# Kernel tuning notes

Measured on AMD Instinct MI355X. Metric: run time of the kernel, lower is better.

Reference implementation:

```python
import jax, jax.numpy as jnp
import numpy as np

BRANCH = 16   # children per internal node
DEPTH = 4     # levels 0..4, leaves at level 4
IN = 512
HID = 512

def _level_sizes():
    return [BRANCH ** d for d in range(DEPTH + 1)]

def setup_inputs() -> dict:
    key = jax.random.key(0)
    ks = jax.random.split(key, 9)
    N = sum(_level_sizes())  # 69905
    x = jax.random.normal(ks[0], (N, IN), dtype=jnp.float32)
    s = 1.0 / np.sqrt(IN + HID)  # torch nn.Linear default init bound
    def lin(kw, kb):
        w = jax.random.uniform(kw, (HID, IN + HID), jnp.float32, -s, s)
        b = jax.random.uniform(kb, (HID,), jnp.float32, -s, s)
        return w, b
    wi_w, wi_b = lin(ks[1], ks[2])
    wf_w, wf_b = lin(ks[3], ks[4])
    wo_w, wo_b = lin(ks[5], ks[6])
    wu_w, wu_b = lin(ks[7], ks[8])
    return {"x": x, "wi_w": wi_w, "wi_b": wi_b, "wf_w": wf_w, "wf_b": wf_b,
            "wo_w": wo_w, "wo_b": wo_b, "wu_w": wu_w, "wu_b": wu_b}

def reference(x, wi_w, wi_b, wf_w, wf_b, wo_w, wo_b, wu_w, wu_b):
    sizes = _level_sizes()
    offs = np.concatenate([[0], np.cumsum(sizes)])
    levels = [x[offs[d]:offs[d + 1]] for d in range(DEPTH + 1)]

    def gates(xh):
        i = jax.nn.sigmoid(xh @ wi_w.T + wi_b)
        o = jax.nn.sigmoid(xh @ wo_w.T + wo_b)
        u = jnp.tanh(xh @ wu_w.T + wu_b)
        return i, o, u

    # leaf_forward: h_prev = 0, no forget terms
    Xl = levels[DEPTH]
    xh = jnp.concatenate([Xl, jnp.zeros((Xl.shape[0], HID), Xl.dtype)], axis=1)
    i, o, u = gates(xh)
    C = i * u
    H = o * jnp.tanh(C)

    # node_forward, bottom-up. Faithful quirk of the source: the forget gate
    # is computed on the child CELL state (cat(x, c_k)), not the hidden state.
    for d in range(DEPTH - 1, -1, -1):
        Xd = levels[d]                      # [n, IN]
        n = Xd.shape[0]
        Hc = H.reshape(n, BRANCH, HID)      # children hidden
        Cc = C.reshape(n, BRANCH, HID)      # children cell
        h_sum = Hc.sum(axis=1)
        xh = jnp.concatenate([Xd, h_sum], axis=1)
        i, o, u = gates(xh)
        xc = jnp.concatenate([jnp.broadcast_to(Xd[:, None, :], (n, BRANCH, IN)), Cc], axis=-1)
        f = jax.nn.sigmoid(jnp.einsum('nbk,hk->nbh', xc, wf_w) + wf_b)
        C = i * u + (f * Cc).sum(axis=1)
        H = o * jnp.tanh(C)

    return H[0], C[0]
```

## Files before the change

### kernel.cpp

```cpp
#include <hip/hip_runtime.h>
#include <stdint.h>
#include <stddef.h>


typedef __bf16 bf16x8 __attribute__((ext_vector_type(8)));
typedef float  f32x4  __attribute__((ext_vector_type(4)));
typedef void __attribute__((address_space(3))) lds_void_t;
typedef void __attribute__((address_space(1))) gbl_void_t;

__device__ __forceinline__ uint16_t f2bf(float f) {
  union { __bf16 b; uint16_t u; } v;
  v.b = (__bf16)f;
  return v.u;
}
__device__ __forceinline__ float bf2f(uint16_t u) {
  union { uint32_t u; float f; } v; v.u = (uint32_t)u << 16;
  return v.f;
}
__device__ __forceinline__ float sig_(float x) {
  return __builtin_amdgcn_rcpf(1.0f + __expf(-x));
}
__device__ __forceinline__ float tanh_(float x) {
  return __builtin_fmaf(2.f,
      __builtin_amdgcn_rcpf(1.f + __expf(-2.f * x)), -1.f);
}

__global__ void k_conv_all(const float4* __restrict__ x,
                           ushort4* __restrict__ xdst, long n4x,
                           const float4* __restrict__ w0,
                           const float4* __restrict__ w1,
                           const float4* __restrict__ w2,
                           const float4* __restrict__ w3,
                           ushort4* __restrict__ wdst) {
  const long per4 = (long)512 * 1024 / 4;
  const long total = n4x + 4 * per4;
  long i = blockIdx.x * (long)blockDim.x + threadIdx.x;
  long stride = (long)gridDim.x * blockDim.x;
  for (; i < total; i += stride) {
    float4 v;
    ushort4* d;
    if (i < n4x) {
      v = x[i];
      d = xdst + i;
    } else {
      long j = i - n4x;
      long seg = j / per4, off2 = j - seg * per4;
      const float4* s = (seg == 0) ? w0 : (seg == 1) ? w1
                       : (seg == 2) ? w2 : w3;
      v = s[off2];
      d = wdst + j;
    }
    ushort4 r;
    r.x = f2bf(v.x); r.y = f2bf(v.y); r.z = f2bf(v.z); r.w = f2bf(v.w);
    *d = r;
  }
}

#define BM 128
#define BN 128
#define BK 32

__global__ __launch_bounds__(256)
void k_gemm_bt(const uint16_t* __restrict__ A, int lda,
               const uint16_t* __restrict__ B, int ldb,
               float* __restrict__ C, int ldc, int K) {
  __shared__ uint16_t As[BM * BK];
  __shared__ uint16_t Bs[BN * BK];
  const int tid = threadIdx.x, lane = tid & 63, wave = tid >> 6;
  const int lrow = lane & 15, quad = lane >> 4;
  const int wm = (wave >> 1) * 64, wn = (wave & 1) * 64;
  const long tm = blockIdx.x, tn = blockIdx.y;
  f32x4 acc[4][4] = {};
  const int srow = lane >> 2, scol = (lane & 3) * 8;
  for (int k0 = 0; k0 < K; k0 += BK) {
#pragma unroll
    for (int i = 0; i < 2; ++i) {
      int row = i * 64 + wave * 16 + srow;
      const uint16_t* gp = A + (tm * BM + row) * (long)lda + k0 + scol;
      __builtin_amdgcn_global_load_lds((gbl_void_t*)(uintptr_t)gp,
          (lds_void_t*)&As[i * 2048 + wave * 512], 16, 0, 0);
    }
#pragma unroll
    for (int i = 0; i < 2; ++i) {
      int row = i * 64 + wave * 16 + srow;
      const uint16_t* gp = B + (tn * BN + row) * (long)ldb + k0 + scol;
      __builtin_amdgcn_global_load_lds((gbl_void_t*)(uintptr_t)gp,
          (lds_void_t*)&Bs[i * 2048 + wave * 512], 16, 0, 0);
    }
    __syncthreads();
    bf16x8 a[4], b[4];
#pragma unroll
    for (int f = 0; f < 4; ++f)
      a[f] = *(const bf16x8*)&As[(wm + f * 16 + lrow) * BK + quad * 8];
#pragma unroll
    for (int f = 0; f < 4; ++f)
      b[f] = *(const bf16x8*)&Bs[(wn + f * 16 + lrow) * BK + quad * 8];
#pragma unroll
    for (int fm = 0; fm < 4; ++fm)
#pragma unroll
      for (int fn = 0; fn < 4; ++fn)
        acc[fm][fn] = __builtin_amdgcn_mfma_f32_16x16x32_bf16(
            a[fm], b[fn], acc[fm][fn], 0, 0, 0);
    __syncthreads();
  }
#pragma unroll
  for (int fm = 0; fm < 4; ++fm)
#pragma unroll
    for (int fn = 0; fn < 4; ++fn) {
      long col  = tn * BN + wn + fn * 16 + lrow;
      long row0 = tm * BM + wm + fm * 16 + quad * 4;
#pragma unroll
      for (int r = 0; r < 4; ++r)
        C[(row0 + r) * (long)ldc + col] = acc[fm][fn][r];
    }
}

template <bool HAS_F>
__global__ __launch_bounds__(256, 3)
void k_level(const uint16_t* __restrict__ A, int lda, int K,
             const uint16_t* __restrict__ Wg,
             const float* __restrict__ bi, const float* __restrict__ bo,
             const float* __restrict__ bu,
             const float* __restrict__ Fpart,
             uint16_t* __restrict__ Cbf,
             const uint16_t* __restrict__ Xnext,
             uint16_t* __restrict__ xh_next) {
  __shared__ uint16_t As[128 * 64];
  __shared__ uint16_t Bs[192 * 64];
  const int tid = threadIdx.x, lane = tid & 63, wave = tid >> 6;
  const int lrow = lane & 15, quad = lane >> 4;
  const int wm = (wave >> 1) * 64, wn = (wave & 1) * 32;

  long tm, tn;
  {
    const int nTm = (int)(gridDim.x >> 3);
    int b = blockIdx.x;
    if ((nTm & 7) == 0) {
      int x = b & 7, j = b >> 3, per = nTm >> 3;
      tn = j & 7; tm = (long)x * per + (j >> 3);
    } else { tm = b >> 3; tn = b & 7; }
  }

  f32x4 acc[3][4][2] = {};

  const int srow = lane >> 3;
  const int scol = (((lane & 7) ^ srow) << 3);
  const int rsw = lrow & 7;
  const int pc[2] = { ((0 + quad) ^ rsw) << 3, ((4 + quad) ^ rsw) << 3 };

  for (int k0 = 0; k0 < K; k0 += 64) {
#pragma unroll
    for (int j = 0; j < 4; ++j) {
      int row = wave * 32 + j * 8 + srow;
      const uint16_t* gp = A + (tm * 128 + row) * (long)lda + k0 + scol;
      __builtin_amdgcn_global_load_lds((gbl_void_t*)(uintptr_t)gp,
          (lds_void_t*)&As[(wave * 32 + j * 8) * 64], 16, 0, 0);
    }
#pragma unroll
    for (int j = 0; j < 6; ++j) {
      int cc = wave * 6 + j;
      int g  = cc >> 3;
      long grow = (long)g * 512 + tn * 64 + (cc & 7) * 8 + srow;
      const uint16_t* gp = Wg + grow * 1024 + k0 + scol;
      __builtin_amdgcn_global_load_lds((gbl_void_t*)(uintptr_t)gp,
          (lds_void_t*)&Bs[cc * 512], 16, 0, 0);
    }
    __syncthreads();

#pragma unroll
    for (int h = 0; h < 2; ++h) {
      bf16x8 a[4];
#pragma unroll
      for (int f = 0; f < 4; ++f)
        a[f] = *(const bf16x8*)&As[(wm + f * 16 + lrow) * 64 + pc[h]];
#pragma unroll
      for (int g = 0; g < 3; ++g) {
        bf16x8 b0 = *(const bf16x8*)&Bs[(g * 64 + wn + lrow) * 64 + pc[h]];
        bf16x8 b1 = *(const bf16x8*)&Bs[(g * 64 + wn + 16 + lrow) * 64 +
                                        pc[h]];
#pragma unroll
        for (int fm = 0; fm < 4; ++fm) {
          acc[g][fm][0] = __builtin_amdgcn_mfma_f32_16x16x32_bf16(
              a[fm], b0, acc[g][fm][0], 0, 0, 0);
          acc[g][fm][1] = __builtin_amdgcn_mfma_f32_16x16x32_bf16(
              a[fm], b1, acc[g][fm][1], 0, 0, 0);
        }
      }
    }
    __syncthreads();
  }

#pragma unroll
  for (int fn = 0; fn < 2; ++fn) {
    long col = tn * 64 + wn + fn * 16 + lrow;
    float biv = bi[col], bov = bo[col], buv = bu[col];
#pragma unroll
    for (int fm = 0; fm < 4; ++fm) {
      long row0 = tm * 128 + wm + fm * 16 + quad * 4;
      long pg   = tm * 8 + (wm >> 4) + fm;
      float hs = 0.f;
#pragma unroll
      for (int r = 0; r < 4; ++r) {
        long row = row0 + r;
        float iv = sig_(acc[0][fm][fn][r] + biv);
        float ov = sig_(acc[1][fm][fn][r] + bov);
        float uv = tanh_(acc[2][fm][fn][r] + buv);
        float c  = iv * uv;
        if (HAS_F) c += Fpart[row * 512 + col];
        Cbf[row * 512 + col] = f2bf(c);
        hs += ov * tanh_(c);
      }
      hs += __shfl_xor(hs, 16, 64);
      hs += __shfl_xor(hs, 32, 64);
      if (quad == 0) {
        xh_next[pg * 1024 + col]       = Xnext[pg * 512 + col];
        xh_next[pg * 1024 + 512 + col] = f2bf(hs);
      }
    }
  }
}

__global__ __launch_bounds__(256, 3)
void k_fc_combine(const uint16_t* __restrict__ Cbf,
                  const uint16_t* __restrict__ Wfc, int ldb,
                  const float* __restrict__ Fx,
                  const float* __restrict__ bfb,
                  float* __restrict__ Fpart) {
  __shared__ uint16_t As[128 * 64];
  __shared__ uint16_t Bs[128 * 64];
  const int tid = threadIdx.x, lane = tid & 63, wave = tid >> 6;
  const int lrow = lane & 15, quad = lane >> 4;
  const int wm = (wave >> 1) * 64, wn = (wave & 1) * 64;
  long tm, tn;
  {
    const int nTm = (int)(gridDim.x >> 2);
    int b = blockIdx.x;
    if ((nTm & 7) == 0) {
      int x = b & 7, j = b >> 3, per = nTm >> 3;
      tn = j & 3; tm = (long)x * per + (j >> 2);
    } else { tm = b >> 2; tn = b & 3; }
  }
  const int lda = 512;
  f32x4 acc[4][4] = {};

  const int srow = lane >> 3;
  const int scol = (((lane & 7) ^ srow) << 3);
  const int rsw = lrow & 7;
  const int pc[2] = { ((0 + quad) ^ rsw) << 3, ((4 + quad) ^ rsw) << 3 };

  for (int k0 = 0; k0 < 512; k0 += 64) {
#pragma unroll
    for (int j = 0; j < 4; ++j) {
      int row = wave * 32 + j * 8 + srow;
      const uint16_t* gp = Cbf + (tm * BM + row) * (long)lda + k0 + scol;
      __builtin_amdgcn_global_load_lds((gbl_void_t*)(uintptr_t)gp,
          (lds_void_t*)&As[(wave * 32 + j * 8) * 64], 16, 0, 0);
    }
#pragma unroll
    for (int j = 0; j < 4; ++j) {
      int row = wave * 32 + j * 8 + srow;
      const uint16_t* gp = Wfc + (tn * BN + row) * (long)ldb + k0 + scol;
      __builtin_amdgcn_global_load_lds((gbl_void_t*)(uintptr_t)gp,
          (lds_void_t*)&Bs[(wave * 32 + j * 8) * 64], 16, 0, 0);
    }
    __syncthreads();
#pragma unroll
    for (int h = 0; h < 2; ++h) {
      bf16x8 a[4], b[4];
#pragma unroll
      for (int f = 0; f < 4; ++f)
        a[f] = *(const bf16x8*)&As[(wm + f * 16 + lrow) * 64 + pc[h]];
#pragma unroll
      for (int f = 0; f < 4; ++f)
        b[f] = *(const bf16x8*)&Bs[(wn + f * 16 + lrow) * 64 + pc[h]];
#pragma unroll
      for (int fm = 0; fm < 4; ++fm)
#pragma unroll
        for (int fn = 0; fn < 4; ++fn)
          acc[fm][fn] = __builtin_amdgcn_mfma_f32_16x16x32_bf16(
              a[fm], b[fn], acc[fm][fn], 0, 0, 0);
    }
    __syncthreads();
  }
#pragma unroll
  for (int fm = 0; fm < 4; ++fm) {
    long pg   = tm * 8 + (wm >> 4) + fm;
    long row0 = tm * BM + wm + fm * 16 + quad * 4;
#pragma unroll
    for (int fn = 0; fn < 4; ++fn) {
      long col = tn * BN + wn + fn * 16 + lrow;
      float fx = Fx[pg * 512 + col] + bfb[col];
      float t = 0.f;
#pragma unroll
      for (int r = 0; r < 4; ++r)
        t += sig_(fx + acc[fm][fn][r]) * bf2f(Cbf[(row0 + r) * 512 + col]);
      t += __shfl_xor(t, 16, 64);
      t += __shfl_xor(t, 32, 64);
      if (quad == 0) Fpart[pg * 512 + col] = t;
    }
  }
}

__global__ void k_dot_bb(const uint16_t* __restrict__ A, int lda,
                         const uint16_t* __restrict__ B, int ldb,
                         float* __restrict__ C, int ldc,
                         int M, int N, int K) {
  int wid  = (int)((blockIdx.x * (long)blockDim.x + threadIdx.x) >> 6);
  int lane = threadIdx.x & 63;
  if (wid >= M * N) return;
  int m = wid / N, n = wid - m * N;
  const uint16_t* a = A + (long)m * lda;
  const uint16_t* b = B + (long)n * ldb;
  int per = K >> 6, k0 = lane * per;
  float s = 0.f;
  for (int j = 0; j < per; j += 4) {
    ushort4 av = *(const ushort4*)(a + k0 + j);
    ushort4 bv = *(const ushort4*)(b + k0 + j);
    s += bf2f(av.x) * bf2f(bv.x) + bf2f(av.y) * bf2f(bv.y)
       + bf2f(av.z) * bf2f(bv.z) + bf2f(av.w) * bf2f(bv.w);
  }
#pragma unroll
  for (int off = 32; off; off >>= 1) s += __shfl_xor(s, off, 64);
  if (lane == 0) C[(long)m * ldc + n] = s;
}
__global__ void k_dot_f32(const float* __restrict__ A, int lda,
                          const float* __restrict__ B, int ldb,
                          float* __restrict__ C, int ldc,
                          int M, int N, int K) {
  int wid  = (int)((blockIdx.x * (long)blockDim.x + threadIdx.x) >> 6);
  int lane = threadIdx.x & 63;
  if (wid >= M * N) return;
  int m = wid / N, n = wid - m * N;
  const float* a = A + (long)m * lda;
  const float* b = B + (long)n * ldb;
  int per = K >> 6, k0 = lane * per;
  float s = 0.f;
  for (int j = 0; j < per; j += 4) {
    float4 av = *(const float4*)(a + k0 + j);
    float4 bv = *(const float4*)(b + k0 + j);
    s += av.x * bv.x + av.y * bv.y + av.z * bv.z + av.w * bv.w;
  }
#pragma unroll
  for (int off = 32; off; off >>= 1) s += __shfl_xor(s, off, 64);
  if (lane == 0) C[(long)m * ldc + n] = s;
}

__global__ void k_hsum_xh4(const float* __restrict__ Hc,
                           const uint16_t* __restrict__ xd,
                           uint16_t* __restrict__ xh, int n) {
  long idx = blockIdx.x * (long)blockDim.x + threadIdx.x;
  if (idx >= (long)n * 128) return;
  long p = idx >> 7; int hq = (int)(idx & 127) << 2;
  const float* hp = Hc + (p << 4) * 512 + hq;
  float4 s = {0.f, 0.f, 0.f, 0.f};
#pragma unroll
  for (int b = 0; b < 16; ++b) {
    float4 v = *(const float4*)(hp + b * 512);
    s.x += v.x; s.y += v.y; s.z += v.z; s.w += v.w;
  }
  *(ushort4*)(xh + p * 1024 + hq) = *(const ushort4*)(xd + p * 512 + hq);
  ushort4 hw = {f2bf(s.x), f2bf(s.y), f2bf(s.z), f2bf(s.w)};
  *(ushort4*)(xh + p * 1024 + 512 + hq) = hw;
}

__global__ void k_final4(const float* __restrict__ G,
                         const float* __restrict__ Fpart,
                         const float* __restrict__ bi,
                         const float* __restrict__ bo,
                         const float* __restrict__ bu,
                         float* __restrict__ H, float* __restrict__ Cv,
                         uint16_t* __restrict__ Cbf, int n) {
  long idx = blockIdx.x * (long)blockDim.x + threadIdx.x;
  if (idx >= (long)n * 128) return;
  long p = idx >> 7; int hq = (int)(idx & 127) << 2;
  const float* g = G + p * 1536;
  float4 gi = *(const float4*)(g + hq);
  float4 go = *(const float4*)(g + 512 + hq);
  float4 gu = *(const float4*)(g + 1024 + hq);
  float4 b_i = *(const float4*)(bi + hq);
  float4 b_o = *(const float4*)(bo + hq);
  float4 b_u = *(const float4*)(bu + hq);
  float4 fp = *(const float4*)(Fpart + p * 512 + hq);
  const float* gip = &gi.x; const float* gop = &go.x; const float* gup = &gu.x;
  const float* bip = &b_i.x; const float* bop = &b_o.x; const float* bup = &b_u.x;
  const float* fpp = &fp.x;
  float4 hv, cv;
  float* hvp = &hv.x; float* cvp = &cv.x;
  ushort4 cw; unsigned short* cwp = &cw.x;
#pragma unroll
  for (int j = 0; j < 4; ++j) {
    float iv = sig_(gip[j] + bip[j]);
    float ov = sig_(gop[j] + bop[j]);
    float uv = tanh_(gup[j] + bup[j]);
    float c  = iv * uv + fpp[j];
    cvp[j] = c;
    cwp[j] = f2bf(c);
    hvp[j] = ov * tanh_(c);
  }
  *(float4*)(H  + p * 512 + hq) = hv;
  *(float4*)(Cv + p * 512 + hq) = cv;
  *(ushort4*)(Cbf + p * 512 + hq) = cw;
}

__global__ void k_root_tail(const float* __restrict__ Fc,
                            const float* __restrict__ Fx,
                            const float* __restrict__ bfb,
                            const float* __restrict__ Cc,
                            const float* __restrict__ G,
                            const float* __restrict__ bi,
                            const float* __restrict__ bo,
                            const float* __restrict__ bu,
                            float* __restrict__ H, float* __restrict__ Cv) {
  int hq = (threadIdx.x & 127) << 2;
  float4 fxv = *(const float4*)(Fx + hq);
  float4 bfv = *(const float4*)(bfb + hq);
  float fx0 = fxv.x + bfv.x, fx1 = fxv.y + bfv.y;
  float fx2 = fxv.z + bfv.z, fx3 = fxv.w + bfv.w;
  float a0 = 0.f, a1 = 0.f, a2 = 0.f, a3 = 0.f;
#pragma unroll 4
  for (int b = 0; b < 16; ++b) {
    float4 f = *(const float4*)(Fc + (long)b * 512 + hq);
    float4 c = *(const float4*)(Cc + (long)b * 512 + hq);
    a0 += sig_(fx0 + f.x) * c.x;
    a1 += sig_(fx1 + f.y) * c.y;
    a2 += sig_(fx2 + f.z) * c.z;
    a3 += sig_(fx3 + f.w) * c.w;
  }
  float fpp[4] = {a0, a1, a2, a3};
  float4 gi = *(const float4*)(G + hq);
  float4 go = *(const float4*)(G + 512 + hq);
  float4 gu = *(const float4*)(G + 1024 + hq);
  float4 b_i = *(const float4*)(bi + hq);
  float4 b_o = *(const float4*)(bo + hq);
  float4 b_u = *(const float4*)(bu + hq);
  const float* gip = &gi.x; const float* gop = &go.x; const float* gup = &gu.x;
  const float* bip = &b_i.x; const float* bop = &b_o.x; const float* bup = &b_u.x;
  float4 hv, cv;
  float* hvp = &hv.x; float* cvp = &cv.x;
#pragma unroll
  for (int j = 0; j < 4; ++j) {
    float iv = sig_(gip[j] + bip[j]);
    float ov = sig_(gop[j] + bop[j]);
    float uv = tanh_(gup[j] + bup[j]);
    float c  = iv * uv + fpp[j];
    cvp[j] = c;
    hvp[j] = ov * tanh_(c);
  }
  *(float4*)(H  + hq) = hv;
  *(float4*)(Cv + hq) = cv;
}

extern "C" void kernel_launch(void* const* d_in, const int* in_sizes, int n_in,
                              void* d_out, int out_size, void* d_ws, size_t ws_size,
                              hipStream_t stream) {
  const float* x    = (const float*)d_in[0];
  const float* wi_w = (const float*)d_in[1];
  const float* wi_b = (const float*)d_in[2];
  const float* wf_w = (const float*)d_in[3];
  const float* wf_b = (const float*)d_in[4];
  const float* wo_w = (const float*)d_in[5];
  const float* wo_b = (const float*)d_in[6];
  const float* wu_w = (const float*)d_in[7];
  const float* wu_b = (const float*)d_in[8];
  (void)in_sizes; (void)n_in; (void)out_size; (void)ws_size;

  static const long offs[5] = {0, 1, 17, 273, 4369};
  const long NTOT = 69905;

  char* ws = (char*)d_ws;
  size_t off = 0;
  auto alloc = [&](size_t bytes) -> void* {
    void* p = ws + off;
    off += (bytes + 255) & ~(size_t)255;
    return p;
  };
  uint16_t* Xbf   = (uint16_t*)alloc(NTOT * 512 * 2);
  uint16_t* Wgw   = (uint16_t*)alloc((size_t)2048 * 1024 * 2);
  uint16_t* Wg    = Wgw;
  uint16_t* Wf    = Wgw + (size_t)1536 * 1024;
  float*    FxAll = (float*)alloc((size_t)4480 * 512 * 4);
  uint16_t* Cbf   = (uint16_t*)alloc((size_t)65536 * 512 * 2);
  uint16_t* CbfU  = (uint16_t*)alloc((size_t)4096 * 512 * 2);
  uint16_t* CbfU2 = (uint16_t*)alloc((size_t)256 * 512 * 2);
  uint16_t* xhA   = (uint16_t*)alloc((size_t)4096 * 1024 * 2);
  uint16_t* xhB   = (uint16_t*)alloc((size_t)256 * 1024 * 2);
  uint16_t* xhC   = (uint16_t*)alloc((size_t)16 * 1024 * 2);
  float*    Fpart = (float*)alloc((size_t)4096 * 512 * 4);
  float*    Gf    = (float*)alloc((size_t)16 * 1536 * 4);
  float*    Fc    = (float*)alloc((size_t)16 * 512 * 4);
  float*    HupA  = (float*)alloc((size_t)16 * 512 * 4);
  float*    CupA  = (float*)alloc((size_t)16 * 512 * 4);

  auto blks = [](long n) { return (int)((n + 255) / 256); };

  {
    long n4x = NTOT * 512 / 4;
    k_conv_all<<<8192, 256, 0, stream>>>(
        (const float4*)x, (ushort4*)Xbf, n4x,
        (const float4*)wi_w, (const float4*)wo_w,
        (const float4*)wu_w, (const float4*)wf_w, (ushort4*)Wgw);
  }

  {
    dim3 grid(35, 4);
    k_gemm_bt<<<grid, 256, 0, stream>>>(Xbf, 512, Wf, 1024, FxAll, 512, 512);
  }

  k_level<false><<<4096, 256, 0, stream>>>(
      Xbf + offs[4] * 512, 512, 512, Wg, wi_b, wo_b, wu_b, nullptr,
      Cbf, Xbf + offs[3] * 512, xhA);
  k_fc_combine<<<2048, 256, 0, stream>>>(Cbf, Wf + 512, 1024,
                                         FxAll + offs[3] * 512, wf_b, Fpart);

  k_level<true><<<256, 256, 0, stream>>>(
      xhA, 1024, 1024, Wg, wi_b, wo_b, wu_b, Fpart,
      CbfU, Xbf + offs[2] * 512, xhB);
  k_fc_combine<<<128, 256, 0, stream>>>(CbfU, Wf + 512, 1024,
                                        FxAll + offs[2] * 512, wf_b, Fpart);

  k_level<true><<<16, 256, 0, stream>>>(
      xhB, 1024, 1024, Wg, wi_b, wo_b, wu_b, Fpart,
      CbfU2, Xbf + offs[1] * 512, xhC);
  k_fc_combine<<<8, 256, 0, stream>>>(CbfU2, Wf + 512, 1024,
                                      FxAll + offs[1] * 512, wf_b, Fpart);

  {
    long waves = 16L * 1536;
    k_dot_bb<<<(int)((waves * 64 + 255) / 256), 256, 0, stream>>>(
        xhC, 1024, Wg, 1024, Gf, 1536, 16, 1536, 1024);
    k_final4<<<blks(16L * 128), 256, 0, stream>>>(
        Gf, Fpart, wi_b, wo_b, wu_b, HupA, CupA, CbfU2, 16);
  }

  k_hsum_xh4<<<1, 256, 0, stream>>>(HupA, Xbf + offs[0] * 512, xhC, 1);
  {
    long waves = 1536;
    k_dot_bb<<<(int)((waves * 64 + 255) / 256), 256, 0, stream>>>(
        xhC, 1024, Wg, 1024, Gf, 1536, 1, 1536, 1024);
  }
  {
    long waves = 16L * 512;
    k_dot_f32<<<(int)((waves * 64 + 255) / 256), 256, 0, stream>>>(
        CupA, 512, wf_w + 512, 1024, Fc, 512, 16, 512, 512);
  }
  k_root_tail<<<1, 128, 0, stream>>>(Fc, FxAll, wf_b, CupA, Gf,
                                     wi_b, wo_b, wu_b,
                                     (float*)d_out, (float*)d_out + 512);
}
```

Before: 518.4 us.

## Halve M-tile for upper tree levels and merge tail kernels

Templates the level and forget-combine GEMM kernels on the M-fragment count, so the small upper levels (levels 2 and 1) use 64-row tiles. That doubles their block counts to fill more CUs. It also fuses the level-1 finalize and hidden-sum into one 1024-thread block that uses LDS, and merges the root gate dot and the Fc dot into one launch. The aim is to cut launch count and raise occupancy in the latency-bound tail, at the cost of less reuse per block of the weight tiles on the small levels.

```diff
diff --git a/kernel.cpp b/kernel.cpp
--- a/kernel.cpp
+++ b/kernel.cpp
@@ -115,7 +115,7 @@
     }
 }
 
-template <bool HAS_F>
+template <bool HAS_F, int MF>
 __global__ __launch_bounds__(256, 3)
 void k_level(const uint16_t* __restrict__ A, int lda, int K,
              const uint16_t* __restrict__ Wg,
@@ -125,11 +125,12 @@
              uint16_t* __restrict__ Cbf,
              const uint16_t* __restrict__ Xnext,
              uint16_t* __restrict__ xh_next) {
-  __shared__ uint16_t As[128 * 64];
+  constexpr int BMT = MF * 32;
+  __shared__ uint16_t As[BMT * 64];
   __shared__ uint16_t Bs[192 * 64];
   const int tid = threadIdx.x, lane = tid & 63, wave = tid >> 6;
   const int lrow = lane & 15, quad = lane >> 4;
-  const int wm = (wave >> 1) * 64, wn = (wave & 1) * 32;
+  const int wm = (wave >> 1) * (MF * 16), wn = (wave & 1) * 32;
 
   long tm, tn;
   {
@@ -141,7 +142,7 @@
     } else { tm = b >> 3; tn = b & 7; }
   }
 
-  f32x4 acc[3][4][2] = {};
+  f32x4 acc[3][MF][2] = {};
 
   const int srow = lane >> 3;
   const int scol = (((lane & 7) ^ srow) << 3);
@@ -150,11 +151,12 @@
 
   for (int k0 = 0; k0 < K; k0 += 64) {
 #pragma unroll
-    for (int j = 0; j < 4; ++j) {
-      int row = wave * 32 + j * 8 + srow;
-      const uint16_t* gp = A + (tm * 128 + row) * (long)lda + k0 + scol;
+    for (int j = 0; j < MF; ++j) {
+      int grp = wave * MF + j;
+      int row = grp * 8 + srow;
+      const uint16_t* gp = A + (tm * BMT + row) * (long)lda + k0 + scol;
       __builtin_amdgcn_global_load_lds((gbl_void_t*)(uintptr_t)gp,
-          (lds_void_t*)&As[(wave * 32 + j * 8) * 64], 16, 0, 0);
+          (lds_void_t*)&As[grp * 512], 16, 0, 0);
     }
 #pragma unroll
     for (int j = 0; j < 6; ++j) {
@@ -169,9 +171,9 @@
 
 #pragma unroll
     for (int h = 0; h < 2; ++h) {
-      bf16x8 a[4];
-#pragma unroll
-      for (int f = 0; f < 4; ++f)
+      bf16x8 a[MF];
+#pragma unroll
+      for (int f = 0; f < MF; ++f)
         a[f] = *(const bf16x8*)&As[(wm + f * 16 + lrow) * 64 + pc[h]];
 #pragma unroll
       for (int g = 0; g < 3; ++g) {
@@ -179,7 +181,7 @@
         bf16x8 b1 = *(const bf16x8*)&Bs[(g * 64 + wn + 16 + lrow) * 64 +
                                         pc[h]];
 #pragma unroll
-        for (int fm = 0; fm < 4; ++fm) {
+        for (int fm = 0; fm < MF; ++fm) {
           acc[g][fm][0] = __builtin_amdgcn_mfma_f32_16x16x32_bf16(
               a[fm], b0, acc[g][fm][0], 0, 0, 0);
           acc[g][fm][1] = __builtin_amdgcn_mfma_f32_16x16x32_bf16(
@@ -195,9 +197,9 @@
     long col = tn * 64 + wn + fn * 16 + lrow;
     float biv = bi[col], bov = bo[col], buv = bu[col];
 #pragma unroll
-    for (int fm = 0; fm < 4; ++fm) {
-      long row0 = tm * 128 + wm + fm * 16 + quad * 4;
-      long pg   = tm * 8 + (wm >> 4) + fm;
+    for (int fm = 0; fm < MF; ++fm) {
+      long row0 = tm * BMT + wm + fm * 16 + quad * 4;
+      long pg   = tm * (BMT / 16) + (wm >> 4) + fm;
       float hs = 0.f;
 #pragma unroll
       for (int r = 0; r < 4; ++r) {
@@ -220,17 +222,19 @@
   }
 }
 
+template <int MF>
 __global__ __launch_bounds__(256, 3)
 void k_fc_combine(const uint16_t* __restrict__ Cbf,
                   const uint16_t* __restrict__ Wfc, int ldb,
                   const float* __restrict__ Fx,
                   const float* __restrict__ bfb,
                   float* __restrict__ Fpart) {
-  __shared__ uint16_t As[128 * 64];
+  constexpr int BMT = MF * 32;
+  __shared__ uint16_t As[BMT * 64];
   __shared__ uint16_t Bs[128 * 64];
   const int tid = threadIdx.x, lane = tid & 63, wave = tid >> 6;
   const int lrow = lane & 15, quad = lane >> 4;
-  const int wm = (wave >> 1) * 64, wn = (wave & 1) * 64;
+  const int wm = (wave >> 1) * (MF * 16), wn = (wave & 1) * 64;
   long tm, tn;
   {
     const int nTm = (int)(gridDim.x >> 2);
@@ -241,7 +245,7 @@
     } else { tm = b >> 2; tn = b & 3; }
   }
   const int lda = 512;
-  f32x4 acc[4][4] = {};
+  f32x4 acc[MF][4] = {};
 
   const int srow = lane >> 3;
   const int scol = (((lane & 7) ^ srow) << 3);
@@ -250,11 +254,12 @@
 
   for (int k0 = 0; k0 < 512; k0 += 64) {
 #pragma unroll
-    for (int j = 0; j < 4; ++j) {
-      int row = wave * 32 + j * 8 + srow;
-      const uint16_t* gp = Cbf + (tm * BM + row) * (long)lda + k0 + scol;
+    for (int j = 0; j < MF; ++j) {
+      int grp = wave * MF + j;
+      int row = grp * 8 + srow;
+      const uint16_t* gp = Cbf + (tm * BMT + row) * (long)lda + k0 + scol;
       __builtin_amdgcn_global_load_lds((gbl_void_t*)(uintptr_t)gp,
-          (lds_void_t*)&As[(wave * 32 + j * 8) * 64], 16, 0, 0);
+          (lds_void_t*)&As[grp * 512], 16, 0, 0);
     }
 #pragma unroll
     for (int j = 0; j < 4; ++j) {
@@ -266,15 +271,15 @@
     __syncthreads();
 #pragma unroll
     for (int h = 0; h < 2; ++h) {
-      bf16x8 a[4], b[4];
-#pragma unroll
-      for (int f = 0; f < 4; ++f)
+      bf16x8 a[MF], b[4];
+#pragma unroll
+      for (int f = 0; f < MF; ++f)
         a[f] = *(const bf16x8*)&As[(wm + f * 16 + lrow) * 64 + pc[h]];
 #pragma unroll
       for (int f = 0; f < 4; ++f)
         b[f] = *(const bf16x8*)&Bs[(wn + f * 16 + lrow) * 64 + pc[h]];
 #pragma unroll
-      for (int fm = 0; fm < 4; ++fm)
+      for (int fm = 0; fm < MF; ++fm)
 #pragma unroll
         for (int fn = 0; fn < 4; ++fn)
           acc[fm][fn] = __builtin_amdgcn_mfma_f32_16x16x32_bf16(
@@ -283,9 +288,9 @@
     __syncthreads();
   }
 #pragma unroll
-  for (int fm = 0; fm < 4; ++fm) {
-    long pg   = tm * 8 + (wm >> 4) + fm;
-    long row0 = tm * BM + wm + fm * 16 + quad * 4;
+  for (int fm = 0; fm < MF; ++fm) {
+    long pg   = tm * (BMT / 16) + (wm >> 4) + fm;
+    long row0 = tm * BMT + wm + fm * 16 + quad * 4;
 #pragma unroll
     for (int fn = 0; fn < 4; ++fn) {
       long col = tn * BN + wn + fn * 16 + lrow;
@@ -323,83 +328,104 @@
   for (int off = 32; off; off >>= 1) s += __shfl_xor(s, off, 64);
   if (lane == 0) C[(long)m * ldc + n] = s;
 }
-__global__ void k_dot_f32(const float* __restrict__ A, int lda,
-                          const float* __restrict__ B, int ldb,
-                          float* __restrict__ C, int ldc,
-                          int M, int N, int K) {
+
+__global__ void k_dot_merge(const uint16_t* __restrict__ xhC,
+                            const uint16_t* __restrict__ Wg,
+                            float* __restrict__ Gf,
+                            const float* __restrict__ CupA,
+                            const float* __restrict__ WfF,
+                            float* __restrict__ Fc) {
   int wid  = (int)((blockIdx.x * (long)blockDim.x + threadIdx.x) >> 6);
   int lane = threadIdx.x & 63;
-  if (wid >= M * N) return;
-  int m = wid / N, n = wid - m * N;
-  const float* a = A + (long)m * lda;
-  const float* b = B + (long)n * ldb;
-  int per = K >> 6, k0 = lane * per;
-  float s = 0.f;
-  for (int j = 0; j < per; j += 4) {
-    float4 av = *(const float4*)(a + k0 + j);
-    float4 bv = *(const float4*)(b + k0 + j);
-    s += av.x * bv.x + av.y * bv.y + av.z * bv.z + av.w * bv.w;
-  }
-#pragma unroll
-  for (int off = 32; off; off >>= 1) s += __shfl_xor(s, off, 64);
-  if (lane == 0) C[(long)m * ldc + n] = s;
-}
-
-__global__ void k_hsum_xh4(const float* __restrict__ Hc,
-                           const uint16_t* __restrict__ xd,
-                           uint16_t* __restrict__ xh, int n) {
-  long idx = blockIdx.x * (long)blockDim.x + threadIdx.x;
-  if (idx >= (long)n * 128) return;
-  long p = idx >> 7; int hq = (int)(idx & 127) << 2;
-  const float* hp = Hc + (p << 4) * 512 + hq;
-  float4 s = {0.f, 0.f, 0.f, 0.f};
-#pragma unroll
-  for (int b = 0; b < 16; ++b) {
-    float4 v = *(const float4*)(hp + b * 512);
-    s.x += v.x; s.y += v.y; s.z += v.z; s.w += v.w;
-  }
-  *(ushort4*)(xh + p * 1024 + hq) = *(const ushort4*)(xd + p * 512 + hq);
-  ushort4 hw = {f2bf(s.x), f2bf(s.y), f2bf(s.z), f2bf(s.w)};
-  *(ushort4*)(xh + p * 1024 + 512 + hq) = hw;
-}
-
-__global__ void k_final4(const float* __restrict__ G,
-                         const float* __restrict__ Fpart,
-                         const float* __restrict__ bi,
-                         const float* __restrict__ bo,
-                         const float* __restrict__ bu,
-                         float* __restrict__ H, float* __restrict__ Cv,
-                         uint16_t* __restrict__ Cbf, int n) {
-  long idx = blockIdx.x * (long)blockDim.x + threadIdx.x;
-  if (idx >= (long)n * 128) return;
-  long p = idx >> 7; int hq = (int)(idx & 127) << 2;
-  const float* g = G + p * 1536;
-  float4 gi = *(const float4*)(g + hq);
-  float4 go = *(const float4*)(g + 512 + hq);
-  float4 gu = *(const float4*)(g + 1024 + hq);
-  float4 b_i = *(const float4*)(bi + hq);
-  float4 b_o = *(const float4*)(bo + hq);
-  float4 b_u = *(const float4*)(bu + hq);
-  float4 fp = *(const float4*)(Fpart + p * 512 + hq);
-  const float* gip = &gi.x; const float* gop = &go.x; const float* gup = &gu.x;
-  const float* bip = &b_i.x; const float* bop = &b_o.x; const float* bup = &b_u.x;
-  const float* fpp = &fp.x;
-  float4 hv, cv;
-  float* hvp = &hv.x; float* cvp = &cv.x;
-  ushort4 cw; unsigned short* cwp = &cw.x;
-#pragma unroll
-  for (int j = 0; j < 4; ++j) {
-    float iv = sig_(gip[j] + bip[j]);
-    float ov = sig_(gop[j] + bop[j]);
-    float uv = tanh_(gup[j] + bup[j]);
-    float c  = iv * uv + fpp[j];
-    cvp[j] = c;
-    cwp[j] = f2bf(c);
-    hvp[j] = ov * tanh_(c);
-  }
-  *(float4*)(H  + p * 512 + hq) = hv;
-  *(float4*)(Cv + p * 512 + hq) = cv;
-  *(ushort4*)(Cbf + p * 512 + hq) = cw;
+  if (wid < 1536) {
+    const uint16_t* a = xhC;
+    const uint16_t* b = Wg + (long)wid * 1024;
+    int k0 = lane * 16;
+    float s = 0.f;
+#pragma unroll
+    for (int j = 0; j < 16; j += 4) {
+      ushort4 av = *(const ushort4*)(a + k0 + j);
+      ushort4 bv = *(const ushort4*)(b + k0 + j);
+      s += bf2f(av.x) * bf2f(bv.x) + bf2f(av.y) * bf2f(bv.y)
+         + bf2f(av.z) * bf2f(bv.z) + bf2f(av.w) * bf2f(bv.w);
+    }
+#pragma unroll
+    for (int off = 32; off; off >>= 1) s += __shfl_xor(s, off, 64);
+    if (lane == 0) Gf[wid] = s;
+  } else {
+    int w2 = wid - 1536;
+    if (w2 >= 16 * 512) return;
+    int m = w2 >> 9, n = w2 & 511;
+    const float* a = CupA + (long)m * 512;
+    const float* b = WfF + (long)n * 1024;
+    int k0 = lane * 8;
+    float s = 0.f;
+#pragma unroll
+    for (int j = 0; j < 8; j += 4) {
+      float4 av = *(const float4*)(a + k0 + j);
+      float4 bv = *(const float4*)(b + k0 + j);
+      s += av.x * bv.x + av.y * bv.y + av.z * bv.z + av.w * bv.w;
+    }
+#pragma unroll
+    for (int off = 32; off; off >>= 1) s += __shfl_xor(s, off, 64);
+    if (lane == 0) Fc[(long)m * 512 + n] = s;
+  }
+}
+
+__global__ __launch_bounds__(1024)
+void k_lvl1_tail(const float* __restrict__ G,
+                 const float* __restrict__ Fpart,
+                 const float* __restrict__ bi,
+                 const float* __restrict__ bo,
+                 const float* __restrict__ bu,
+                 float* __restrict__ Cv,
+                 const uint16_t* __restrict__ xroot,
+                 uint16_t* __restrict__ xh) {
+  __shared__ float Hl[16 * 512];
+  const int tid = threadIdx.x;
+#pragma unroll
+  for (int it = 0; it < 2; ++it) {
+    int idx = it * 1024 + tid;
+    int p = idx >> 7, hq = (idx & 127) << 2;
+    const float* g = G + (long)p * 1536;
+    float4 gi = *(const float4*)(g + hq);
+    float4 go = *(const float4*)(g + 512 + hq);
+    float4 gu = *(const float4*)(g + 1024 + hq);
+    float4 b_i = *(const float4*)(bi + hq);
+    float4 b_o = *(const float4*)(bo + hq);
+    float4 b_u = *(const float4*)(bu + hq);
+    float4 fp = *(const float4*)(Fpart + (long)p * 512 + hq);
+    const float* gip = &gi.x; const float* gop = &go.x;
+    const float* gup = &gu.x; const float* bip = &b_i.x;
+    const float* bop = &b_o.x; const float* bup = &b_u.x;
+    const float* fpp = &fp.x;
+    float4 hv, cv;
+    float* hvp = &hv.x; float* cvp = &cv.x;
+#pragma unroll
+    for (int j = 0; j < 4; ++j) {
+      float iv = sig_(gip[j] + bip[j]);
+      float ov = sig_(gop[j] + bop[j]);
+      float uv = tanh_(gup[j] + bup[j]);
+      float c  = iv * uv + fpp[j];
+      cvp[j] = c;
+      hvp[j] = ov * tanh_(c);
+    }
+    *(float4*)(Cv + (long)p * 512 + hq) = cv;
+    *(float4*)(&Hl[p * 512 + hq]) = hv;
+  }
+  __syncthreads();
+  if (tid < 128) {
+    int hq = tid << 2;
+    float4 s = {0.f, 0.f, 0.f, 0.f};
+#pragma unroll
+    for (int b = 0; b < 16; ++b) {
+      float4 v = *(const float4*)(&Hl[b * 512 + hq]);
+      s.x += v.x; s.y += v.y; s.z += v.z; s.w += v.w;
+    }
+    *(ushort4*)(xh + hq) = *(const ushort4*)(xroot + hq);
+    ushort4 hw = {f2bf(s.x), f2bf(s.y), f2bf(s.z), f2bf(s.w)};
+    *(ushort4*)(xh + 512 + hq) = hw;
+  }
 }
 
 __global__ void k_root_tail(const float* __restrict__ Fc,
@@ -488,10 +514,7 @@
   float*    Fpart = (float*)alloc((size_t)4096 * 512 * 4);
   float*    Gf    = (float*)alloc((size_t)16 * 1536 * 4);
   float*    Fc    = (float*)alloc((size_t)16 * 512 * 4);
-  float*    HupA  = (float*)alloc((size_t)16 * 512 * 4);
   float*    CupA  = (float*)alloc((size_t)16 * 512 * 4);
-
-  auto blks = [](long n) { return (int)((n + 255) / 256); };
 
   {
     long n4x = NTOT * 512 / 4;
@@ -506,42 +529,36 @@
     k_gemm_bt<<<grid, 256, 0, stream>>>(Xbf, 512, Wf, 1024, FxAll, 512, 512);
   }
 
-  k_level<false><<<4096, 256, 0, stream>>>(
+  k_level<false, 4><<<4096, 256, 0, stream>>>(
       Xbf + offs[4] * 512, 512, 512, Wg, wi_b, wo_b, wu_b, nullptr,
       Cbf, Xbf + offs[3] * 512, xhA);
-  k_fc_combine<<<2048, 256, 0, stream>>>(Cbf, Wf + 512, 1024,
-                                         FxAll + offs[3] * 512, wf_b, Fpart);
-
-  k_level<true><<<256, 256, 0, stream>>>(
+  k_fc_combine<4><<<2048, 256, 0, stream>>>(Cbf, Wf + 512, 1024,
+                                            FxAll + offs[3] * 512, wf_b, Fpart);
+
+  k_level<true, 2><<<512, 256, 0, stream>>>(
       xhA, 1024, 1024, Wg, wi_b, wo_b, wu_b, Fpart,
       CbfU, Xbf + offs[2] * 512, xhB);
-  k_fc_combine<<<128, 256, 0, stream>>>(CbfU, Wf + 512, 1024,
-                                        FxAll + offs[2] * 512, wf_b, Fpart);
-
-  k_level<true><<<16, 256, 0, stream>>>(
+  k_fc_combine<2><<<256, 256, 0, stream>>>(CbfU, Wf + 512, 1024,
+                                           FxAll + offs[2] * 512, wf_b, Fpart);
+
+  k_level<true, 2><<<32, 256, 0, stream>>>(
       xhB, 1024, 1024, Wg, wi_b, wo_b, wu_b, Fpart,
       CbfU2, Xbf + offs[1] * 512, xhC);
-  k_fc_combine<<<8, 256, 0, stream>>>(CbfU2, Wf + 512, 1024,
-                                      FxAll + offs[1] * 512, wf_b, Fpart);
+  k_fc_combine<2><<<16, 256, 0, stream>>>(CbfU2, Wf + 512, 1024,
+                                          FxAll + offs[1] * 512, wf_b, Fpart);
 
   {
     long waves = 16L * 1536;
     k_dot_bb<<<(int)((waves * 64 + 255) / 256), 256, 0, stream>>>(
         xhC, 1024, Wg, 1024, Gf, 1536, 16, 1536, 1024);
-    k_final4<<<blks(16L * 128), 256, 0, stream>>>(
-        Gf, Fpart, wi_b, wo_b, wu_b, HupA, CupA, CbfU2, 16);
-  }
-
-  k_hsum_xh4<<<1, 256, 0, stream>>>(HupA, Xbf + offs[0] * 512, xhC, 1);
+    k_lvl1_tail<<<1, 1024, 0, stream>>>(Gf, Fpart, wi_b, wo_b, wu_b,
+                                        CupA, Xbf + offs[0] * 512, xhC);
+  }
+
   {
-    long waves = 1536;
-    k_dot_bb<<<(int)((waves * 64 + 255) / 256), 256, 0, stream>>>(
-        xhC, 1024, Wg, 1024, Gf, 1536, 1, 1536, 1024);
-  }
-  {
-    long waves = 16L * 512;
-    k_dot_f32<<<(int)((waves * 64 + 255) / 256), 256, 0, stream>>>(
-        CupA, 512, wf_w + 512, 1024, Fc, 512, 16, 512, 512);
+    long waves = 1536 + 16L * 512;
+    k_dot_merge<<<(int)(waves / 4), 256, 0, stream>>>(
+        xhC, Wg, Gf, CupA, wf_w + 512, Fc);
   }
   k_root_tail<<<1, 128, 0, stream>>>(Fc, FxAll, wf_b, CupA, Gf,
                                      wi_b, wo_b, wu_b,
```

New measurement: 494.9 us. -4.5%, faster.
